# Optimization experiments

Measured on AMD Instinct MI355X. Metric: run time of the kernel, lower is better.

Reference implementation:

```python
import jax, jax.numpy as jnp
import numpy as np

N = 50000
E = 800000
IN_FEATS = 128
HID = 64   # per-head hidden dim
OUT = 64   # per-head out dim
H = 4      # num heads
SLOPE = 0.2


def setup_inputs() -> dict:
    key = jax.random.key(0)
    ks = jax.random.split(key, 10)
    feat = jax.random.normal(ks[0], (N, IN_FEATS), dtype=jnp.float32)
    src = jax.random.randint(ks[1], (E,), 0, N, dtype=jnp.int32)
    # every node gets exactly E//N incoming edges -> no zero in-degree
    dst = (jnp.arange(E, dtype=jnp.int32) % N).astype(jnp.int32)
    s1 = 1.0 / np.sqrt(IN_FEATS)
    s2 = 1.0 / np.sqrt(HID)
    W1 = jax.random.normal(ks[2], (IN_FEATS, H * HID), dtype=jnp.float32) * s1
    al1 = jax.random.normal(ks[3], (H, HID), dtype=jnp.float32) * s2
    ar1 = jax.random.normal(ks[4], (H, HID), dtype=jnp.float32) * s2
    b1 = jnp.zeros((H * HID,), dtype=jnp.float32)
    W2 = jax.random.normal(ks[5], (HID, H * OUT), dtype=jnp.float32) * s2
    al2 = jax.random.normal(ks[6], (H, OUT), dtype=jnp.float32) * (1.0 / np.sqrt(OUT))
    ar2 = jax.random.normal(ks[7], (H, OUT), dtype=jnp.float32) * (1.0 / np.sqrt(OUT))
    b2 = jnp.zeros((H * OUT,), dtype=jnp.float32)
    return {"feat": feat, "src": src, "dst": dst,
            "W1": W1, "al1": al1, "ar1": ar1, "b1": b1,
            "W2": W2, "al2": al2, "ar2": ar2, "b2": b2}


def gat_conv(x, src, dst, W, al, ar, b, n_heads, d_head):
    # x: (N, F_in) -> h: (N, H, Dh)
    h = (x @ W).reshape(-1, n_heads, d_head)
    el = jnp.sum(h * al[None], axis=-1)  # (N, H)
    er = jnp.sum(h * ar[None], axis=-1)  # (N, H)
    e = jax.nn.leaky_relu(el[src] + er[dst], negative_slope=SLOPE)  # (E, H)
    # edge-softmax over incoming edges of each dst node
    m = jax.ops.segment_max(e, dst, num_segments=N)           # (N, H)
    ex = jnp.exp(e - m[dst])                                   # (E, H)
    denom = jax.ops.segment_sum(ex, dst, num_segments=N)       # (N, H)
    alpha = ex / denom[dst]                                    # (E, H)
    msg = h[src] * alpha[:, :, None]                           # (E, H, Dh)
    out = jax.ops.segment_sum(msg, dst, num_segments=N)        # (N, H, Dh)
    return out + b.reshape(1, n_heads, d_head)


def reference(feat, src, dst, W1, al1, ar1, b1, W2, al2, ar2, b2):
    h = gat_conv(feat, src, dst, W1, al1, ar1, b1, H, HID).mean(axis=1)  # head-mean
    out = gat_conv(h, src, dst, W2, al2, ar2, b2, H, OUT).mean(axis=1)
    return out  # (N, OUT)
```

## Files before the change

### kernel.cpp

```cpp
#include <hip/hip_runtime.h>
#include <hip/hip_fp16.h>


#define NNODES 50000

typedef __attribute__((ext_vector_type(8))) short short8v;
typedef __attribute__((ext_vector_type(4))) float f32x4;

__device__ __forceinline__ unsigned short bf16_rne(float x) {
  union { float f; unsigned u; } v;
  v.f = x;
  unsigned r = v.u + 0x7FFF + ((v.u >> 16) & 1);
  return (unsigned short)(r >> 16);
}
__device__ __forceinline__ float bf16_f(unsigned short h) {
  union { unsigned u; float f; } v;
  v.u = ((unsigned)h) << 16;
  return v.f;
}
__device__ __forceinline__ float rl_f(float x, int lane) {
  return __int_as_float(__builtin_amdgcn_readlane(__float_as_int(x), lane));
}

__global__ __launch_bounds__(256) void xcast_kernel(
    const float* __restrict__ X, __half* __restrict__ Xh, int n4) {
  const int t = blockIdx.x * 256 + threadIdx.x;
  if (t >= n4) return;
  const float4 v = reinterpret_cast<const float4*>(X)[t];
  ushort4 o;
  o.x = __half_as_ushort(__float2half(v.x));
  o.y = __half_as_ushort(__float2half(v.y));
  o.z = __half_as_ushort(__float2half(v.z));
  o.w = __half_as_ushort(__float2half(v.w));
  reinterpret_cast<ushort4*>(Xh)[t] = o;
}

__global__ void prep_kernel(const float* __restrict__ W1, const float* __restrict__ al1,
                            const float* __restrict__ ar1, const float* __restrict__ b1,
                            const float* __restrict__ W2, const float* __restrict__ al2,
                            const float* __restrict__ ar2, const float* __restrict__ b2,
                            float* __restrict__ P) {
  const int t = blockIdx.x * 256 + threadIdx.x;
  if (t < 512) {
    const int k = t >> 2, h = t & 3;
    float s = 0.f;
    for (int c = 0; c < 64; ++c) s = fmaf(W1[k * 256 + h * 64 + c], al1[h * 64 + c], s);
    P[t] = s;
  } else if (t < 1024) {
    const int u = t - 512, k = u >> 2, h = u & 3;
    float s = 0.f;
    for (int c = 0; c < 64; ++c) s = fmaf(W1[k * 256 + h * 64 + c], ar1[h * 64 + c], s);
    P[t] = s;
  } else if (t < 1280) {
    const int u = t - 1024, k = u >> 2, h = u & 3;
    float s = 0.f;
    for (int c = 0; c < 64; ++c) s = fmaf(W2[k * 256 + h * 64 + c], al2[h * 64 + c], s);
    P[t] = s;
  } else if (t < 1536) {
    const int u = t - 1280, k = u >> 2, h = u & 3;
    float s = 0.f;
    for (int c = 0; c < 64; ++c) s = fmaf(W2[k * 256 + h * 64 + c], ar2[h * 64 + c], s);
    P[t] = s;
  } else if (t < 1600) {
    const int c = t - 1536;
    P[t] = 0.25f * (b1[c] + b1[64 + c] + b1[128 + c] + b1[192 + c]);
  } else if (t < 1664) {
    const int c = t - 1600;
    P[t] = 0.25f * (b2[c] + b2[64 + c] + b2[128 + c] + b2[192 + c]);
  }
}

__global__ void prep_wfrag(const float* __restrict__ W1, const float* __restrict__ W2,
                           unsigned short* __restrict__ whi1, unsigned short* __restrict__ wlo1,
                           unsigned short* __restrict__ whi2, unsigned short* __restrict__ wlo2) {
  const int t = blockIdx.x * 256 + threadIdx.x;
  if (t < 32768) {
    const int j = t & 7, lane = (t >> 3) & 63, ct = (t >> 9) & 3;
    const int ks = (t >> 11) & 7, hf = (t >> 14) & 1;
    const int kl = ks * 32 + ((lane >> 4) << 3) + j;
    const int h = kl >> 6, fl = kl & 63;
    const int c = ct * 16 + (lane & 15);
    const float w = W1[(hf * 64 + fl) * 256 + h * 64 + c];
    const unsigned short hi = bf16_rne(w);
    whi1[t] = hi;
    wlo1[t] = bf16_rne(w - bf16_f(hi));
  } else if (t < 49152) {
    const int u = t - 32768;
    const int j = u & 7, lane = (u >> 3) & 63, ct = (u >> 9) & 3;
    const int ks = (u >> 11) & 7;
    const int kl = ks * 32 + ((lane >> 4) << 3) + j;
    const int h = kl >> 6, fl = kl & 63;
    const int c = ct * 16 + (lane & 15);
    const float w = W2[fl * 256 + h * 64 + c];
    const unsigned short hi = bf16_rne(w);
    whi2[u] = hi;
    wlo2[u] = bf16_rne(w - bf16_f(hi));
  }
}

template <int F>
__global__ __launch_bounds__(256) void attcoef_kernel(
    const __half* __restrict__ X, const float* __restrict__ wal,
    const float* __restrict__ war, float* __restrict__ el, float* __restrict__ er,
    int N) {
  __shared__ float4 WL[F], WR[F];
  const int tid = threadIdx.x;
  for (int i = tid; i < F; i += 256) {
    WL[i] = reinterpret_cast<const float4*>(wal)[i];
    WR[i] = reinterpret_cast<const float4*>(war)[i];
  }
  __syncthreads();
  const int row = blockIdx.x * 256 + tid;
  if (row >= N) return;
  const __half* __restrict__ xr = X + (size_t)row * F;
  float accl[4] = {0, 0, 0, 0}, accr[4] = {0, 0, 0, 0};
  for (int k = 0; k < F; k += 4) {
    const ushort4 u4 = *reinterpret_cast<const ushort4*>(xr + k);
    const float xs[4] = {__half2float(__ushort_as_half(u4.x)),
                         __half2float(__ushort_as_half(u4.y)),
                         __half2float(__ushort_as_half(u4.z)),
                         __half2float(__ushort_as_half(u4.w))};
#pragma unroll
    for (int kk = 0; kk < 4; ++kk) {
      const float4 wl = WL[k + kk], wr = WR[k + kk];
      accl[0] = fmaf(xs[kk], wl.x, accl[0]);
      accl[1] = fmaf(xs[kk], wl.y, accl[1]);
      accl[2] = fmaf(xs[kk], wl.z, accl[2]);
      accl[3] = fmaf(xs[kk], wl.w, accl[3]);
      accr[0] = fmaf(xs[kk], wr.x, accr[0]);
      accr[1] = fmaf(xs[kk], wr.y, accr[1]);
      accr[2] = fmaf(xs[kk], wr.z, accr[2]);
      accr[3] = fmaf(xs[kk], wr.w, accr[3]);
    }
  }
  float4 o;
  o.x = accl[0]; o.y = accl[1]; o.z = accl[2]; o.w = accl[3];
  *reinterpret_cast<float4*>(el + (size_t)row * 4) = o;
  o.x = accr[0]; o.y = accr[1]; o.z = accr[2]; o.w = accr[3];
  *reinterpret_cast<float4*>(er + (size_t)row * 4) = o;
}

template <int F, typename OT>
__global__ __launch_bounds__(256) void fused_gat_mfma(
    const __half* __restrict__ X, const float* __restrict__ el,
    const float* __restrict__ er, const int* __restrict__ src,
    const unsigned short* __restrict__ whif, const unsigned short* __restrict__ wlof,
    const float* __restrict__ bavg, OT* __restrict__ out, int N) {
  constexpr int NHALF = F / 64;
  __shared__ unsigned Ghi[16 * 128];
  __shared__ unsigned Glo[16 * 128];

  const int tid = threadIdx.x;
  const int lane = tid & 63;
  const int wv = tid >> 6;
  const int base = blockIdx.x * 16;

  const int ka = lane & 15;
  const int ha = lane >> 4;
  float areg[4];
  int sreg[4];
#pragma unroll
  for (int i = 0; i < 4; ++i) {
    int v = base + wv * 4 + i;
    if (v > N - 1) v = N - 1;
    const int s = src[v + ka * N];
    sreg[i] = s;
    float e = el[(size_t)s * 4 + ha] + er[(size_t)v * 4 + ha];
    e = (e > 0.f) ? e : 0.2f * e;
    float m = e;
#pragma unroll
    for (int d = 1; d < 16; d <<= 1) m = fmaxf(m, __shfl_xor(m, d, 16));
    const float ex = __expf(e - m);
    float den = ex;
#pragma unroll
    for (int d = 1; d < 16; d <<= 1) den += __shfl_xor(den, d, 16);
    areg[i] = ex / den;
  }

  const int an = lane & 15;
  const int aq = lane >> 4;
  const int swzr = (an & 7) << 2;
  f32x4 acc = {0.f, 0.f, 0.f, 0.f};

  unsigned short* GhiU = reinterpret_cast<unsigned short*>(Ghi);
  unsigned short* GloU = reinterpret_cast<unsigned short*>(Glo);

#pragma unroll 1
  for (int hf = 0; hf < NHALF; ++hf) {
    if (hf) __syncthreads();
#pragma unroll
    for (int i = 0; i < 4; ++i) {
      const int nodeL = wv * 4 + i;
      float s0 = 0, s1 = 0, s2 = 0, s3 = 0;
#pragma unroll
      for (int k = 0; k < 16; ++k) {
        const int sk = __builtin_amdgcn_readlane(sreg[i], k);
        const float v0 = rl_f(areg[i], k);
        const float v1 = rl_f(areg[i], k + 16);
        const float v2 = rl_f(areg[i], k + 32);
        const float v3 = rl_f(areg[i], k + 48);
        const float x = __half2float(X[(size_t)sk * F + hf * 64 + lane]);
        s0 = fmaf(v0, x, s0);
        s1 = fmaf(v1, x, s1);
        s2 = fmaf(v2, x, s2);
        s3 = fmaf(v3, x, s3);
      }
      const int swz = (nodeL & 7) << 2;
      const float av[4] = {s0, s1, s2, s3};
#pragma unroll
      for (int h = 0; h < 4; ++h) {
        const int kl = h * 64 + lane;
        const int us = (((kl >> 1) ^ swz) << 1) + (kl & 1);
        const unsigned short hi = bf16_rne(av[h]);
        GhiU[nodeL * 256 + us] = hi;
        GloU[nodeL * 256 + us] = bf16_rne(av[h] - bf16_f(hi));
      }
    }
    __syncthreads();

#pragma unroll
    for (int s = 0; s < 8; ++s) {
      const int uo = an * 128 + ((s * 16 + aq * 4) ^ swzr);
      const short8v ahi = *reinterpret_cast<const short8v*>(&Ghi[uo]);
      const short8v alo = *reinterpret_cast<const short8v*>(&Glo[uo]);
      const size_t fo = (((size_t)(hf * 8 + s) * 4 + wv) * 64 + lane) * 8;
      const short8v bh = *reinterpret_cast<const short8v*>(whif + fo);
      const short8v bl = *reinterpret_cast<const short8v*>(wlof + fo);
      acc = __builtin_amdgcn_mfma_f32_16x16x32_bf16(ahi, bh, acc, 0, 0, 0);
      acc = __builtin_amdgcn_mfma_f32_16x16x32_bf16(alo, bh, acc, 0, 0, 0);
      acc = __builtin_amdgcn_mfma_f32_16x16x32_bf16(ahi, bl, acc, 0, 0, 0);
    }
  }

  const int cc = lane & 15;
  const int r0 = (lane >> 4) * 4;
  const int c0 = wv * 16;
  const float bv = bavg[c0 + cc];
#pragma unroll
  for (int j = 0; j < 4; ++j) {
    const int r = base + r0 + j;
    if (r < N) {
      const float val = 0.25f * acc[j] + bv;
      if constexpr (sizeof(OT) == 2) {
        out[(size_t)r * 64 + c0 + cc] = __float2half(val);
      } else {
        out[(size_t)r * 64 + c0 + cc] = val;
      }
    }
  }
}

extern "C" void kernel_launch(void* const* d_in, const int* in_sizes, int n_in,
                              void* d_out, int out_size, void* d_ws,
                              size_t ws_size, hipStream_t stream) {
  const float* feat = (const float*)d_in[0];
  const int* src = (const int*)d_in[1];
  const float* W1 = (const float*)d_in[3];
  const float* al1 = (const float*)d_in[4];
  const float* ar1 = (const float*)d_in[5];
  const float* b1 = (const float*)d_in[6];
  const float* W2 = (const float*)d_in[7];
  const float* al2 = (const float*)d_in[8];
  const float* ar2 = (const float*)d_in[9];
  const float* b2 = (const float*)d_in[10];
  float* out = (float*)d_out;

  const int N = NNODES;

  char* base = (char*)d_ws;
  float* Pf = (float*)base;
  unsigned short* whi1 = (unsigned short*)(base + 8192);
  unsigned short* wlo1 = whi1 + 32768;
  unsigned short* whi2 = wlo1 + 32768;
  unsigned short* wlo2 = whi2 + 16384;
  float* el = (float*)(base + 262144);
  float* er = el + (size_t)N * 4;
  __half* Xh = (__half*)(er + (size_t)N * 4);
  __half* x2h = Xh + (size_t)N * 128;

  float* wal1 = Pf;
  float* war1 = Pf + 512;
  float* wal2 = Pf + 1024;
  float* war2 = Pf + 1280;
  float* bavg1 = Pf + 1536;
  float* bavg2 = Pf + 1600;

  prep_kernel<<<7, 256, 0, stream>>>(W1, al1, ar1, b1, W2, al2, ar2, b2, Pf);
  prep_wfrag<<<192, 256, 0, stream>>>(W1, W2, whi1, wlo1, whi2, wlo2);
  const int n4 = N * 128 / 4;
  xcast_kernel<<<(n4 + 255) / 256, 256, 0, stream>>>(feat, Xh, n4);

  const int rowBlocks = (N + 255) / 256;
  const int tileBlocks = (N + 15) / 16;

  attcoef_kernel<128><<<rowBlocks, 256, 0, stream>>>(Xh, wal1, war1, el, er, N);
  fused_gat_mfma<128, __half>
      <<<tileBlocks, 256, 0, stream>>>(Xh, el, er, src, whi1, wlo1, bavg1, x2h, N);

  attcoef_kernel<64><<<rowBlocks, 256, 0, stream>>>(x2h, wal2, war2, el, er, N);
  fused_gat_mfma<64, float>
      <<<tileBlocks, 256, 0, stream>>>(x2h, el, er, src, whi2, wlo2, bavg2, out, N);
}
```

Baseline: 119.9 us.

## Switch aggregate-then-project MFMA from split bf16 to fp16 with single-term A

Replaces the bf16 hi/lo split with fp16 for the weights and drops the low part of the aggregated features, so each k-step issues two f16 MFMAs instead of three bf16 ones. For the 128-feature layer, both feature halves are gathered at once with half2 loads into one shared buffer, which removes the inner half loop and its extra barrier. This cuts MFMA count, shared-memory traffic and gather instructions, but lowers the precision of the aggregated activations to plain fp16.

```diff
diff --git a/kernel.cpp b/kernel.cpp
--- a/kernel.cpp
+++ b/kernel.cpp
@@ -4,22 +4,15 @@
 
 #define NNODES 50000
 
-typedef __attribute__((ext_vector_type(8))) short short8v;
+typedef __attribute__((ext_vector_type(8))) _Float16 half8v;
 typedef __attribute__((ext_vector_type(4))) float f32x4;
 
-__device__ __forceinline__ unsigned short bf16_rne(float x) {
-  union { float f; unsigned u; } v;
-  v.f = x;
-  unsigned r = v.u + 0x7FFF + ((v.u >> 16) & 1);
-  return (unsigned short)(r >> 16);
-}
-__device__ __forceinline__ float bf16_f(unsigned short h) {
-  union { unsigned u; float f; } v;
-  v.u = ((unsigned)h) << 16;
-  return v.f;
-}
 __device__ __forceinline__ float rl_f(float x, int lane) {
   return __int_as_float(__builtin_amdgcn_readlane(__float_as_int(x), lane));
+}
+__device__ __forceinline__ unsigned pack_h2(float a, float b) {
+  return (unsigned)__half_as_ushort(__float2half(a)) |
+         ((unsigned)__half_as_ushort(__float2half(b)) << 16);
 }
 
 __global__ __launch_bounds__(256) void xcast_kernel(
@@ -75,26 +68,25 @@
                            unsigned short* __restrict__ whi2, unsigned short* __restrict__ wlo2) {
   const int t = blockIdx.x * 256 + threadIdx.x;
   if (t < 32768) {
-    const int j = t & 7, lane = (t >> 3) & 63, ct = (t >> 9) & 3;
-    const int ks = (t >> 11) & 7, hf = (t >> 14) & 1;
-    const int kl = ks * 32 + ((lane >> 4) << 3) + j;
-    const int h = kl >> 6, fl = kl & 63;
+    const int j = t & 7, lane = (t >> 3) & 63, ct = (t >> 9) & 3, s = t >> 11;
+    const int k = s * 32 + ((lane >> 4) << 3) + j;
+    const int hf = k >> 8, rem = k & 255;
+    const int h = rem >> 6, fl = rem & 63;
     const int c = ct * 16 + (lane & 15);
     const float w = W1[(hf * 64 + fl) * 256 + h * 64 + c];
-    const unsigned short hi = bf16_rne(w);
-    whi1[t] = hi;
-    wlo1[t] = bf16_rne(w - bf16_f(hi));
+    const __half hi = __float2half(w);
+    whi1[t] = __half_as_ushort(hi);
+    wlo1[t] = __half_as_ushort(__float2half(w - __half2float(hi)));
   } else if (t < 49152) {
     const int u = t - 32768;
-    const int j = u & 7, lane = (u >> 3) & 63, ct = (u >> 9) & 3;
-    const int ks = (u >> 11) & 7;
-    const int kl = ks * 32 + ((lane >> 4) << 3) + j;
-    const int h = kl >> 6, fl = kl & 63;
+    const int j = u & 7, lane = (u >> 3) & 63, ct = (u >> 9) & 3, s = u >> 11;
+    const int k = s * 32 + ((lane >> 4) << 3) + j;
+    const int h = k >> 6, fl = k & 63;
     const int c = ct * 16 + (lane & 15);
     const float w = W2[fl * 256 + h * 64 + c];
-    const unsigned short hi = bf16_rne(w);
-    whi2[u] = hi;
-    wlo2[u] = bf16_rne(w - bf16_f(hi));
+    const __half hi = __float2half(w);
+    whi2[u] = __half_as_ushort(hi);
+    wlo2[u] = __half_as_ushort(__float2half(w - __half2float(hi)));
   }
 }
 
@@ -146,9 +138,8 @@
     const float* __restrict__ er, const int* __restrict__ src,
     const unsigned short* __restrict__ whif, const unsigned short* __restrict__ wlof,
     const float* __restrict__ bavg, OT* __restrict__ out, int N) {
-  constexpr int NHALF = F / 64;
-  __shared__ unsigned Ghi[16 * 128];
-  __shared__ unsigned Glo[16 * 128];
+  constexpr int DPR = F * 2;
+  __shared__ unsigned Gp[16 * DPR];
 
   const int tid = threadIdx.x;
   const int lane = tid & 63;
@@ -177,17 +168,37 @@
     areg[i] = ex / den;
   }
 
-  const int an = lane & 15;
-  const int aq = lane >> 4;
-  const int swzr = (an & 7) << 2;
-  f32x4 acc = {0.f, 0.f, 0.f, 0.f};
-
-  unsigned short* GhiU = reinterpret_cast<unsigned short*>(Ghi);
-  unsigned short* GloU = reinterpret_cast<unsigned short*>(Glo);
-
-#pragma unroll 1
-  for (int hf = 0; hf < NHALF; ++hf) {
-    if (hf) __syncthreads();
+  if constexpr (F == 128) {
+    const int hf = lane >> 5;
+    const int l31 = lane & 31;
+#pragma unroll
+    for (int i = 0; i < 4; ++i) {
+      const int nodeL = wv * 4 + i;
+      float2 sh0{0, 0}, sh1{0, 0}, sh2{0, 0}, sh3{0, 0};
+#pragma unroll
+      for (int k = 0; k < 16; ++k) {
+        const int sk = __builtin_amdgcn_readlane(sreg[i], k);
+        const float a0 = rl_f(areg[i], k);
+        const float a1 = rl_f(areg[i], k + 16);
+        const float a2 = rl_f(areg[i], k + 32);
+        const float a3 = rl_f(areg[i], k + 48);
+        const __half2 x2 = *reinterpret_cast<const __half2*>(X + (size_t)sk * 128 + lane * 2);
+        const float2 xf = __half22float2(x2);
+        sh0.x = fmaf(a0, xf.x, sh0.x); sh0.y = fmaf(a0, xf.y, sh0.y);
+        sh1.x = fmaf(a1, xf.x, sh1.x); sh1.y = fmaf(a1, xf.y, sh1.y);
+        sh2.x = fmaf(a2, xf.x, sh2.x); sh2.y = fmaf(a2, xf.y, sh2.y);
+        sh3.x = fmaf(a3, xf.x, sh3.x); sh3.y = fmaf(a3, xf.y, sh3.y);
+      }
+      const int swz = (nodeL & 7) << 2;
+      const float2 av[4] = {sh0, sh1, sh2, sh3};
+#pragma unroll
+      for (int h = 0; h < 4; ++h) {
+        const int d = hf * 128 + h * 32 + l31;
+        Gp[nodeL * DPR + (d ^ swz)] = pack_h2(av[h].x, av[h].y);
+      }
+    }
+  } else {
+    unsigned short* GU = reinterpret_cast<unsigned short*>(Gp);
 #pragma unroll
     for (int i = 0; i < 4; ++i) {
       const int nodeL = wv * 4 + i;
@@ -199,7 +210,7 @@
         const float v1 = rl_f(areg[i], k + 16);
         const float v2 = rl_f(areg[i], k + 32);
         const float v3 = rl_f(areg[i], k + 48);
-        const float x = __half2float(X[(size_t)sk * F + hf * 64 + lane]);
+        const float x = __half2float(X[(size_t)sk * 64 + lane]);
         s0 = fmaf(v0, x, s0);
         s1 = fmaf(v1, x, s1);
         s2 = fmaf(v2, x, s2);
@@ -209,27 +220,28 @@
       const float av[4] = {s0, s1, s2, s3};
 #pragma unroll
       for (int h = 0; h < 4; ++h) {
-        const int kl = h * 64 + lane;
-        const int us = (((kl >> 1) ^ swz) << 1) + (kl & 1);
-        const unsigned short hi = bf16_rne(av[h]);
-        GhiU[nodeL * 256 + us] = hi;
-        GloU[nodeL * 256 + us] = bf16_rne(av[h] - bf16_f(hi));
+        const int dw = (h * 32 + (lane >> 1)) ^ swz;
+        GU[nodeL * (2 * DPR) + dw * 2 + (lane & 1)] =
+            __half_as_ushort(__float2half(av[h]));
       }
     }
-    __syncthreads();
-
-#pragma unroll
-    for (int s = 0; s < 8; ++s) {
-      const int uo = an * 128 + ((s * 16 + aq * 4) ^ swzr);
-      const short8v ahi = *reinterpret_cast<const short8v*>(&Ghi[uo]);
-      const short8v alo = *reinterpret_cast<const short8v*>(&Glo[uo]);
-      const size_t fo = (((size_t)(hf * 8 + s) * 4 + wv) * 64 + lane) * 8;
-      const short8v bh = *reinterpret_cast<const short8v*>(whif + fo);
-      const short8v bl = *reinterpret_cast<const short8v*>(wlof + fo);
-      acc = __builtin_amdgcn_mfma_f32_16x16x32_bf16(ahi, bh, acc, 0, 0, 0);
-      acc = __builtin_amdgcn_mfma_f32_16x16x32_bf16(alo, bh, acc, 0, 0, 0);
-      acc = __builtin_amdgcn_mfma_f32_16x16x32_bf16(ahi, bl, acc, 0, 0, 0);
-    }
+  }
+  __syncthreads();
+
+  const int an = lane & 15;
+  const int aq = lane >> 4;
+  const int swzr = (an & 7) << 2;
+  f32x4 acc = {0.f, 0.f, 0.f, 0.f};
+
+#pragma unroll
+  for (int s = 0; s < F / 8; ++s) {
+    const int dbase = an * DPR + ((s * 16 + aq * 4) ^ swzr);
+    const half8v ah = *reinterpret_cast<const half8v*>(&Gp[dbase]);
+    const size_t fo = (((size_t)s * 4 + wv) * 64 + lane) * 8;
+    const half8v bh = *reinterpret_cast<const half8v*>(whif + fo);
+    const half8v bl = *reinterpret_cast<const half8v*>(wlof + fo);
+    acc = __builtin_amdgcn_mfma_f32_16x16x32_f16(ah, bh, acc, 0, 0, 0);
+    acc = __builtin_amdgcn_mfma_f32_16x16x32_f16(ah, bl, acc, 0, 0, 0);
   }
 
   const int cc = lane & 15;
```

Measured after the change: 103.5 us. 1.16x faster.
